# Optimization experiments

Hardware: AMD Instinct MI355X
Metric: run time of the kernel (lower is better)

Reference implementation:

```python
import jax, jax.numpy as jnp
import numpy as np

EPS = 1e-5

def _ln(t, w, b):
    m = t.mean(-1, keepdims=True)
    xc = t - m
    var = (xc * xc).mean(-1, keepdims=True)
    return xc * jax.lax.rsqrt(var + EPS) * w + b

def _rope(q, k, cos, sin):
    # q,k: [B,H,N,hd]; cos,sin: [N, hd//2]
    def rot(t):
        B, H, N, hd = t.shape
        tp = t.reshape(B, H, N, hd // 2, 2)
        r, i = tp[..., 0], tp[..., 1]
        c = cos[None, None, :, :]
        s = sin[None, None, :, :]
        orr = r * c - i * s
        oii = r * s + i * c
        return jnp.stack([orr, oii], axis=-1).reshape(B, H, N, hd)
    return rot(q), rot(k)

def setup_inputs() -> dict:
    key = jax.random.key(0)
    B, N1, N2, D, H = 2, 2048, 256, 1024, 16
    hd = D // H
    ks = jax.random.split(key, 8)
    def w(k, shape):
        return jax.random.normal(k, shape, jnp.float32) * 0.02
    x = jax.random.normal(ks[0], (B, N1, D), jnp.float32)
    c = jax.random.normal(ks[1], (B, N2, D), jnp.float32)
    # rotary tables
    t = jnp.arange(N1, dtype=jnp.float32)
    inv_freq = 1.0 / (10000.0 ** (jnp.arange(0, hd, 2, dtype=jnp.float32) / hd))
    ang = jnp.outer(t, inv_freq)  # [N1, hd//2]
    return dict(
        x=x, c=c,
        freqs_cos=jnp.cos(ang), freqs_sin=jnp.sin(ang),
        W_qkv1=w(ks[2], (D, 3 * D)), b_qkv1=jnp.zeros(3 * D, jnp.float32),
        W_qkv2=w(ks[3], (D, 3 * D)), b_qkv2=jnp.zeros(3 * D, jnp.float32),
        qn1_w=jnp.ones(hd, jnp.float32), qn1_b=jnp.zeros(hd, jnp.float32),
        kn1_w=jnp.ones(hd, jnp.float32), kn1_b=jnp.zeros(hd, jnp.float32),
        qn2_w=jnp.ones(hd, jnp.float32), qn2_b=jnp.zeros(hd, jnp.float32),
        kn2_w=jnp.ones(hd, jnp.float32), kn2_b=jnp.zeros(hd, jnp.float32),
        W_proj1=w(ks[4], (D, D)), b_proj1=jnp.zeros(D, jnp.float32),
        W_proj2=w(ks[5], (D, D)), b_proj2=jnp.zeros(D, jnp.float32),
        pre_x=0,
    )

def reference(x, c, freqs_cos, freqs_sin,
              W_qkv1, b_qkv1, W_qkv2, b_qkv2,
              qn1_w, qn1_b, kn1_w, kn1_b,
              qn2_w, qn2_b, kn2_w, kn2_b,
              W_proj1, b_proj1, W_proj2, b_proj2, pre_x):
    B, N1, D = x.shape
    N2 = c.shape[1]
    H = 16
    hd = D // H
    scale = hd ** -0.5

    def split_heads(qkv):
        q, k, v = jnp.split(qkv, 3, axis=-1)
        f = lambda t: t.reshape(B, -1, H, hd).transpose(0, 2, 1, 3)
        return f(q), f(k), f(v)

    q1, k1, v1 = split_heads(x @ W_qkv1 + b_qkv1)
    q1 = _ln(q1, qn1_w, qn1_b)
    k1 = _ln(k1, kn1_w, kn1_b)
    if pre_x:
        qr, kr = _rope(q1[:, :, pre_x:], k1[:, :, pre_x:], freqs_cos, freqs_sin)
        q1 = jnp.concatenate([q1[:, :, :pre_x], qr], axis=2)
        k1 = jnp.concatenate([k1[:, :, :pre_x], kr], axis=2)
    else:
        q1, k1 = _rope(q1, k1, freqs_cos, freqs_sin)

    q2, k2, v2 = split_heads(c @ W_qkv2 + b_qkv2)
    q2 = _ln(q2, qn2_w, qn2_b)
    k2 = _ln(k2, kn2_w, kn2_b)

    q = jnp.concatenate([q1, q2], axis=2)
    k = jnp.concatenate([k1, k2], axis=2)
    v = jnp.concatenate([v1, v2], axis=2)

    scores = jnp.einsum('bhqd,bhkd->bhqk', q, k) * scale
    attn = jax.nn.softmax(scores, axis=-1)
    o = jnp.einsum('bhqk,bhkd->bhqd', attn, v)  # [B,H,N,hd]
    o = o.transpose(0, 2, 1, 3).reshape(B, N1 + N2, D)

    x_out = o[:, :N1] @ W_proj1 + b_proj1
    c_out = o[:, N1:] @ W_proj2 + b_proj2
    return (x_out, c_out)
```

## Files before the change

### kernel.cpp

```cpp
#include <hip/hip_runtime.h>
#include <hip/hip_bf16.h>
#include <stdint.h>

typedef __attribute__((ext_vector_type(8))) short short8;
typedef __attribute__((ext_vector_type(4))) short bf4;
typedef __attribute__((ext_vector_type(4))) float f32x4;

#define B_ 2
#define N1 2048
#define N2 256
#define NT 2304
#define D_ 1024
#define H_ 16
#define HD 64
#define QSCALE 0.18033688011112042f
#define RESCALE_THR 8.0f

static __device__ __forceinline__ float bf2f(short s){
  union { unsigned int u; float f; } u;
  u.u = ((unsigned int)(unsigned short)s) << 16;
  return u.f;
}
static __device__ __forceinline__ short f2bf(float f){
  union { float f; unsigned int u; } v; v.f = f;
  unsigned int u = v.u;
  unsigned int lsb = (u >> 16) & 1u;
  u += 0x7fffu + lsb;
  return (short)(u >> 16);
}
static __device__ __forceinline__ unsigned int cvtpk2(float a, float b){
  union { __hip_bfloat162 h; unsigned int u; } cv;
  cv.h = __float22bfloat162_rn(make_float2(a, b));
  return cv.u;
}

static __device__ __forceinline__ float fexp2(float x){
#if __has_builtin(__builtin_amdgcn_exp2f)
  return __builtin_amdgcn_exp2f(x);
#else
  return exp2f(x);
#endif
}

static __device__ __forceinline__ void gload16(const void* g, void* l){
  __builtin_amdgcn_global_load_lds(
      (const __attribute__((address_space(1))) void*)g,
      (__attribute__((address_space(3))) void*)l, 16, 0, 0);
}

static __device__ __forceinline__ int swz(int row, int chunk){
  return (row << 6) + ((chunk ^ (row & 7)) << 3);
}

__global__ __launch_bounds__(256) void k_cvt_all(const float* __restrict__ x,
                                                 const float* __restrict__ c,
                                                 short* __restrict__ out){
  int i = (blockIdx.x * 256 + threadIdx.x) * 8;
  const float* in = (i < 4194304) ? (x + i) : (c + (i - 4194304));
  float4 a = *(const float4*)(in);
  float4 b = *(const float4*)(in + 4);
  short8 o;
  o[0]=f2bf(a.x); o[1]=f2bf(a.y); o[2]=f2bf(a.z); o[3]=f2bf(a.w);
  o[4]=f2bf(b.x); o[5]=f2bf(b.y); o[6]=f2bf(b.z); o[7]=f2bf(b.w);
  *(short8*)(out + i) = o;
}

__global__ __launch_bounds__(256) void k_transpose_w4(
    const float* __restrict__ Wq1, const float* __restrict__ Wq2,
    const float* __restrict__ Wp1, const float* __restrict__ Wp2,
    short* __restrict__ Wt1, short* __restrict__ Wt2,
    short* __restrict__ Wtp1, short* __restrict__ Wtp2){
  const int id = blockIdx.x;
  const float* W; short* Wt; int N; int bx, by;
  if (id < 768)      { W = Wq1; Wt = Wt1;  N = 3072; bx = id % 48;          by = id / 48; }
  else if (id < 1536){ W = Wq2; Wt = Wt2;  N = 3072; bx = (id-768) % 48;    by = (id-768) / 48; }
  else if (id < 1792){ W = Wp1; Wt = Wtp1; N = 1024; bx = (id-1536) % 16;   by = (id-1536) / 16; }
  else               { W = Wp2; Wt = Wtp2; N = 1024; bx = (id-1792) % 16;   by = (id-1792) / 16; }
  const int K = 1024;
  __shared__ float tl[64][65];
  const int n0 = bx * 64, k0 = by * 64;
  const int t = threadIdx.x, r = t >> 2, c = (t & 3) * 16;
  const float* src = W + (size_t)(k0 + r) * N + n0 + c;
  #pragma unroll
  for (int i = 0; i < 16; i += 4){
    float4 v = *(const float4*)(src + i);
    tl[r][c+i] = v.x; tl[r][c+i+1] = v.y; tl[r][c+i+2] = v.z; tl[r][c+i+3] = v.w;
  }
  __syncthreads();
  short8 o0, o1;
  #pragma unroll
  for (int i = 0; i < 8; i++) o0[i] = f2bf(tl[c+i][r]);
  #pragma unroll
  for (int i = 0; i < 8; i++) o1[i] = f2bf(tl[c+8+i][r]);
  short* dst = Wt + (size_t)(n0 + r) * K + k0 + c;
  *(short8*)(dst)     = o0;
  *(short8*)(dst + 8) = o1;
}

template<int OUT_BF16>
__global__ __launch_bounds__(256) void k_gemm_bt(const short* __restrict__ A,
                                                 const short* __restrict__ Bt,
                                                 const short* __restrict__ Bt2,
                                                 const float* __restrict__ bias,
                                                 const float* __restrict__ bias2,
                                                 void* __restrict__ Cp,
                                                 int N, int K, int Msplit){
  __shared__ __align__(16) short As[128*32];
  __shared__ __align__(16) short Bs[128*32];
  const int t = threadIdx.x;
  const int w = t >> 6, l = t & 63;
  const int lc = l & 15, g = l >> 4;
  const int gx = gridDim.x;
  const int nb = gx * gridDim.y;
  const int bid = blockIdx.y * gx + blockIdx.x;
  const int nbid = (bid & 7) * (nb >> 3) + (bid >> 3);
  const int tm = (nbid / gx) * 128, tn = (nbid % gx) * 128;
  const int wm = (w >> 1) * 64, wn = (w & 1) * 64;

  const short* Bsel = (tm < Msplit) ? Bt : Bt2;
  const float* bsel = (tm < Msplit) ? bias : bias2;

  const int r0 = w*32 + (l >> 2);
  const int r1 = r0 + 16;
  const int cb = (l & 3) * 16;

  const char* Ag0 = (const char*)(A + (size_t)(tm + r0) * K) + cb;
  const char* Ag1 = (const char*)(A + (size_t)(tm + r1) * K) + cb;
  const char* Bg0 = (const char*)(Bsel + (size_t)(tn + r0) * K) + cb;
  const char* Bg1 = (const char*)(Bsel + (size_t)(tn + r1) * K) + cb;
  char* Al0 = (char*)As + (w*2  )*1024;
  char* Al1 = (char*)As + (w*2+1)*1024;
  char* Bl0 = (char*)Bs + (w*2  )*1024;
  char* Bl1 = (char*)Bs + (w*2+1)*1024;

  f32x4 acc[4][4];
  #pragma unroll
  for (int m=0;m<4;m++){
    #pragma unroll
    for (int n=0;n<4;n++){ acc[m][n][0]=0.f; acc[m][n][1]=0.f; acc[m][n][2]=0.f; acc[m][n][3]=0.f; }
  }

  for (int k0 = 0; k0 < K; k0 += 32){
    const int kb = k0 * 2;
    gload16(Ag0 + kb, Al0);
    gload16(Ag1 + kb, Al1);
    gload16(Bg0 + kb, Bl0);
    gload16(Bg1 + kb, Bl1);
    __syncthreads();
    short8 af[4], bfr[4];
    #pragma unroll
    for (int m=0;m<4;m++) af[m]  = *(const short8*)(As + (wm + m*16 + lc)*32 + g*8);
    #pragma unroll
    for (int n=0;n<4;n++) bfr[n] = *(const short8*)(Bs + (wn + n*16 + lc)*32 + g*8);
    #pragma unroll
    for (int m=0;m<4;m++){
      #pragma unroll
      for (int n=0;n<4;n++)
        acc[m][n] = __builtin_amdgcn_mfma_f32_16x16x32_bf16(af[m], bfr[n], acc[m][n], 0, 0, 0);
    }
    __syncthreads();
  }

  #pragma unroll
  for (int n=0;n<4;n++){
    const int col = tn + wn + n*16 + lc;
    const float bv = bsel[col];
    #pragma unroll
    for (int m=0;m<4;m++){
      const int row = tm + wm + m*16 + g*4;
      #pragma unroll
      for (int r=0;r<4;r++){
        float v = acc[m][n][r] + bv;
        if (OUT_BF16) ((short*)Cp)[(size_t)(row + r)*N + col] = f2bf(v);
        else          ((float*)Cp)[(size_t)(row + r)*N + col] = v;
      }
    }
  }
}

__global__ __launch_bounds__(256) void k_lnrope(const short* __restrict__ qkv,
    const float* __restrict__ qw, const float* __restrict__ qb,
    const float* __restrict__ kw, const float* __restrict__ kb,
    const float* __restrict__ fcos, const float* __restrict__ fsin,
    short* __restrict__ Qo, short* __restrict__ Ko, short* __restrict__ Vo,
    int Nseq, int posoff, int use_rope){
  const int wv = (blockIdx.x * 256 + threadIdx.x) >> 6;
  const int l = threadIdx.x & 63;
  const int h = wv % H_;
  const int n = (wv / H_) % Nseq;
  const int b = wv / (H_ * Nseq);
  const size_t ibase = ((size_t)(b * Nseq + n)) * 3072 + h * 64 + l;
  float q = bf2f(qkv[ibase]);
  float k = bf2f(qkv[ibase + 1024]);
  short v = qkv[ibase + 2048];

  float mu = q;
  #pragma unroll
  for (int mk = 1; mk < 64; mk <<= 1) mu += __shfl_xor(mu, mk, 64);
  mu *= (1.f/64.f);
  float dq = q - mu;
  float var = dq * dq;
  #pragma unroll
  for (int mk = 1; mk < 64; mk <<= 1) var += __shfl_xor(var, mk, 64);
  var *= (1.f/64.f);
  float qn = dq * rsqrtf(var + 1e-5f) * qw[l] + qb[l];

  float muk = k;
  #pragma unroll
  for (int mk = 1; mk < 64; mk <<= 1) muk += __shfl_xor(muk, mk, 64);
  muk *= (1.f/64.f);
  float dk = k - muk;
  float vark = dk * dk;
  #pragma unroll
  for (int mk = 1; mk < 64; mk <<= 1) vark += __shfl_xor(vark, mk, 64);
  vark *= (1.f/64.f);
  float kn = dk * rsqrtf(vark + 1e-5f) * kw[l] + kb[l];

  if (use_rope){
    float cv = fcos[(size_t)n * 32 + (l >> 1)];
    float sv = fsin[(size_t)n * 32 + (l >> 1)];
    float qp = __shfl_xor(qn, 1, 64);
    float kp = __shfl_xor(kn, 1, 64);
    qn = (l & 1) ? (qp * sv + qn * cv) : (qn * cv - qp * sv);
    kn = (l & 1) ? (kp * sv + kn * cv) : (kn * cv - kp * sv);
  }
  qn *= QSCALE;
  const size_t obase = ((size_t)(b * H_ + h) * NT + posoff + n) * HD + l;
  Qo[obase] = f2bf(qn);
  Ko[obase] = f2bf(kn);
  Vo[obase] = v;
}

__global__ __launch_bounds__(256) void k_transpose_v(const short* __restrict__ V,
                                                     short* __restrict__ Vt){
  __shared__ short tl[64][72];
  const int blk = blockIdx.x;
  const int bh = blk / 36;
  const int n0 = (blk % 36) * 64;
  const int t = threadIdx.x, r = t >> 2, c = (t & 3) * 16;
  const short* src = V + ((size_t)bh * NT + n0 + r) * HD + c;
  short8 v0 = *(const short8*)(src);
  short8 v1 = *(const short8*)(src + 8);
  #pragma unroll
  for (int i=0;i<8;i++){ tl[r][c+i] = v0[i]; tl[r][c+8+i] = v1[i]; }
  __syncthreads();
  short8 o0, o1;
  #pragma unroll
  for (int i=0;i<8;i++){ o0[i] = tl[c+i][r]; o1[i] = tl[c+8+i][r]; }
  short* dst = Vt + ((size_t)bh * HD + r) * NT + n0 + c;
  *(short8*)dst       = o0;
  *(short8*)(dst + 8) = o1;
}

__global__ __launch_bounds__(512) void k_attn(const short* __restrict__ Q,
                                              const short* __restrict__ Kg,
                                              const short* __restrict__ Vt,
                                              short* __restrict__ o1,
                                              short* __restrict__ o2){
  __shared__ __align__(16) short Kl[2][4096];
  __shared__ __align__(16) short Vl[2][4096];
  __shared__ __align__(16) short Ps[8][1024];
  const int t = threadIdx.x, w = t >> 6, l = t & 63;
  const int lc = l & 15, g = l >> 4;
  const int blk = blockIdx.x;
  const int ch = blk & 7, ii = blk >> 3;
  const int bh = ch * 4 + (ii / 18);
  const int qt = ii % 18;
  const int b = bh >> 4, hh = bh & 15;
  const int q0 = qt * 128 + w * 16;
  const short* Qb = Q  + (size_t)bh * NT * HD;
  const short* Kb = Kg + (size_t)bh * NT * HD;
  const short* Vb = Vt + (size_t)bh * HD * NT;

  short8 qf0 = *(const short8*)(Qb + (size_t)(q0 + lc) * HD + g*8);
  short8 qf1 = *(const short8*)(Qb + (size_t)(q0 + lc) * HD + g*8 + 32);

  const int sr = t >> 3, c0 = t & 7;
  const short* Kgp = Kb + (size_t)sr * HD + c0 * 8;
  const short* Vgp = Vb + (size_t)sr * NT + c0 * 8;
  const int w0 = swz(sr, c0);

  float mcur = -1e30f, lcur = 0.f;
  f32x4 oacc[4];
  #pragma unroll
  for (int j=0;j<4;j++){ oacc[j][0]=0.f; oacc[j][1]=0.f; oacc[j][2]=0.f; oacc[j][3]=0.f; }

  {
    short8 k0 = *(const short8*)(Kgp);
    short8 v0 = *(const short8*)(Vgp);
    *(short8*)&Kl[0][w0] = k0;
    *(short8*)&Vl[0][w0] = v0;
  }
  __syncthreads();

  for (int ti = 0; ti < 36; ++ti){
    const int cur = ti & 1;
    short8 kn0, vn0;
    if (ti < 35){
      kn0 = *(const short8*)(Kgp + (size_t)(ti + 1) * 64 * HD);
      vn0 = *(const short8*)(Vgp + (ti + 1) * 64);
    }
    f32x4 s[4];
    __builtin_amdgcn_s_setprio(1);
    #pragma unroll
    for (int j=0;j<4;j++){
      const int row = j*16 + lc;
      short8 k0 = *(const short8*)(&Kl[cur][swz(row, g)]);
      short8 k1 = *(const short8*)(&Kl[cur][swz(row, g + 4)]);
      f32x4 a; a[0]=0.f; a[1]=0.f; a[2]=0.f; a[3]=0.f;
      a = __builtin_amdgcn_mfma_f32_16x16x32_bf16(k0, qf0, a, 0, 0, 0);
      a = __builtin_amdgcn_mfma_f32_16x16x32_bf16(k1, qf1, a, 0, 0, 0);
      s[j] = a;
    }
    __builtin_amdgcn_s_setprio(0);
    float t0 = fmaxf(fmaxf(s[0][0], s[0][1]), fmaxf(s[0][2], s[0][3]));
    float t1 = fmaxf(fmaxf(s[1][0], s[1][1]), fmaxf(s[1][2], s[1][3]));
    float t2 = fmaxf(fmaxf(s[2][0], s[2][1]), fmaxf(s[2][2], s[2][3]));
    float t3 = fmaxf(fmaxf(s[3][0], s[3][1]), fmaxf(s[3][2], s[3][3]));
    float tmx = fmaxf(fmaxf(t0, t1), fmaxf(t2, t3));
    tmx = fmaxf(tmx, __shfl_xor(tmx, 16, 64));
    tmx = fmaxf(tmx, __shfl_xor(tmx, 32, 64));
    float mn = mcur;
    if (__any(tmx > mcur + RESCALE_THR)){
      mn = fmaxf(mcur, tmx);
      const float fsc = fexp2(mcur - mn);
      mcur = mn;
      lcur *= fsc;
      #pragma unroll
      for (int j=0;j<4;j++){
        oacc[j][0] *= fsc; oacc[j][1] *= fsc; oacc[j][2] *= fsc; oacc[j][3] *= fsc;
      }
    }
    float p[4][4];
    #pragma unroll
    for (int j=0;j<4;j++){
      p[j][0] = fexp2(s[j][0] - mn);
      p[j][1] = fexp2(s[j][1] - mn);
      p[j][2] = fexp2(s[j][2] - mn);
      p[j][3] = fexp2(s[j][3] - mn);
    }
    float rs = ((p[0][0]+p[0][1])+(p[0][2]+p[0][3]))
             + ((p[1][0]+p[1][1])+(p[1][2]+p[1][3]))
             + ((p[2][0]+p[2][1])+(p[2][2]+p[2][3]))
             + ((p[3][0]+p[3][1])+(p[3][2]+p[3][3]));
    rs += __shfl_xor(rs, 16, 64);
    rs += __shfl_xor(rs, 32, 64);
    lcur += rs;
    #pragma unroll
    for (int j=0;j<4;j++){
      const int si = (lc << 6) + (((2*j + (g >> 1)) ^ (lc & 7)) << 3) + (g & 1) * 4;
      unsigned int* dst = (unsigned int*)&Ps[w][si];
      dst[0] = cvtpk2(p[j][0], p[j][1]);
      dst[1] = cvtpk2(p[j][2], p[j][3]);
    }
    #pragma unroll
    for (int kk=0;kk<2;kk++){
      short8 pa = *(const short8*)(&Ps[w][swz(lc, 4*kk + g)]);
      __builtin_amdgcn_s_setprio(1);
      #pragma unroll
      for (int jd=0;jd<4;jd++){
        short8 vb = *(const short8*)(&Vl[cur][swz(lc + 16*jd, 4*kk + g)]);
        oacc[jd] = __builtin_amdgcn_mfma_f32_16x16x32_bf16(vb, pa, oacc[jd], 0, 0, 0);
      }
      __builtin_amdgcn_s_setprio(0);
    }
    if (ti < 35){
      *(short8*)&Kl[cur ^ 1][w0] = kn0;
      *(short8*)&Vl[cur ^ 1][w0] = vn0;
    }
    __syncthreads();
  }

  const float inv = 1.0f / lcur;
  const int qi = q0 + lc;
  short* obase = (qi < N1) ? (o1 + ((size_t)b * N1 + qi) * D_)
                           : (o2 + ((size_t)b * N2 + (qi - N1)) * D_);
  #pragma unroll
  for (int jd=0;jd<4;jd++){
    bf4 ov;
    #pragma unroll
    for (int r=0;r<4;r++) ov[r] = f2bf(oacc[jd][r] * inv);
    *(bf4*)(obase + hh*64 + 16*jd + 4*g) = ov;
  }
}

extern "C" void kernel_launch(void* const* d_in, const int* in_sizes, int n_in,
                              void* d_out, int out_size, void* d_ws, size_t ws_size,
                              hipStream_t stream){
  const float* x    = (const float*)d_in[0];
  const float* c    = (const float*)d_in[1];
  const float* fc   = (const float*)d_in[2];
  const float* fs   = (const float*)d_in[3];
  const float* Wq1  = (const float*)d_in[4];
  const float* bq1  = (const float*)d_in[5];
  const float* Wq2  = (const float*)d_in[6];
  const float* bq2  = (const float*)d_in[7];
  const float* qn1w = (const float*)d_in[8];
  const float* qn1b = (const float*)d_in[9];
  const float* kn1w = (const float*)d_in[10];
  const float* kn1b = (const float*)d_in[11];
  const float* qn2w = (const float*)d_in[12];
  const float* qn2b = (const float*)d_in[13];
  const float* kn2w = (const float*)d_in[14];
  const float* kn2b = (const float*)d_in[15];
  const float* Wp1  = (const float*)d_in[16];
  const float* bp1  = (const float*)d_in[17];
  const float* Wp2  = (const float*)d_in[18];
  const float* bp2  = (const float*)d_in[19];
  float* out = (float*)d_out;

  char* ws = (char*)d_ws;
  short* xb   = (short*)(ws);
  short* Wt1  = (short*)(ws + 9437184);
  short* Wt2  = (short*)(ws + 15728640);
  short* Wtp1 = (short*)(ws + 22020096);
  short* Wtp2 = (short*)(ws + 24117248);
  short* qkv1 = (short*)(ws + 26214400);
  short* qkv2 = (short*)(ws + 51380224);
  short* Qb   = (short*)(ws + 54525952);
  short* Kb   = (short*)(ws + 63963136);
  short* Vb   = (short*)(ws + 73400320);
  short* o1   = (short*)(ws + 26214400);
  short* Vtb  = (short*)(ws + 26214400 + 9437184);

  k_cvt_all<<<2304, 256, 0, stream>>>(x, c, xb);
  k_transpose_w4<<<2048, 256, 0, stream>>>(Wq1, Wq2, Wp1, Wp2, Wt1, Wt2, Wtp1, Wtp2);

  k_gemm_bt<1><<<dim3(24,36), 256, 0, stream>>>(xb, Wt1, Wt2, bq1, bq2, qkv1, 3072, 1024, 4096);

  k_lnrope<<<16384, 256, 0, stream>>>(qkv1, qn1w, qn1b, kn1w, kn1b, fc, fs, Qb, Kb, Vb, 2048, 0, 1);
  k_lnrope<<<2048,  256, 0, stream>>>(qkv2, qn2w, qn2b, kn2w, kn2b, fc, fs, Qb, Kb, Vb,  256, 2048, 0);

  k_transpose_v<<<1152, 256, 0, stream>>>(Vb, Vtb);
  k_attn<<<576, 512, 0, stream>>>(Qb, Kb, Vtb, o1, o1 + 4194304);

  k_gemm_bt<0><<<dim3(8,36), 256, 0, stream>>>(o1, Wtp1, Wtp2, bp1, bp2, out, 1024, 1024, 4096);
}
```

Before: 217.1 us.

## Fuse per-head LayerNorm, RoPE and V transpose into QKV GEMM epilogue

```diff
diff --git a/kernel.cpp b/kernel.cpp
--- a/kernel.cpp
+++ b/kernel.cpp
@@ -97,14 +97,15 @@
   *(short8*)(dst + 8) = o1;
 }
 
-template<int OUT_BF16>
-__global__ __launch_bounds__(256) void k_gemm_bt(const short* __restrict__ A,
-                                                 const short* __restrict__ Bt,
-                                                 const short* __restrict__ Bt2,
-                                                 const float* __restrict__ bias,
-                                                 const float* __restrict__ bias2,
-                                                 void* __restrict__ Cp,
-                                                 int N, int K, int Msplit){
+__global__ __launch_bounds__(256) void k_gemm_qkv(const short* __restrict__ A,
+    const short* __restrict__ Bt, const short* __restrict__ Bt2,
+    const float* __restrict__ bias, const float* __restrict__ bias2,
+    const float* __restrict__ qn1w, const float* __restrict__ qn1b,
+    const float* __restrict__ kn1w, const float* __restrict__ kn1b,
+    const float* __restrict__ qn2w, const float* __restrict__ qn2b,
+    const float* __restrict__ kn2w, const float* __restrict__ kn2b,
+    const float* __restrict__ fcos, const float* __restrict__ fsin,
+    short* __restrict__ Qo, short* __restrict__ Ko, short* __restrict__ Vto){
   __shared__ __align__(16) short As[128*32];
   __shared__ __align__(16) short Bs[128*32];
   const int t = threadIdx.x;
@@ -116,9 +117,11 @@
   const int nbid = (bid & 7) * (nb >> 3) + (bid >> 3);
   const int tm = (nbid / gx) * 128, tn = (nbid % gx) * 128;
   const int wm = (w >> 1) * 64, wn = (w & 1) * 64;
-
-  const short* Bsel = (tm < Msplit) ? Bt : Bt2;
-  const float* bsel = (tm < Msplit) ? bias : bias2;
+  const int K = 1024;
+  const bool s1 = (tm < 4096);
+
+  const short* Bsel = s1 ? Bt : Bt2;
+  const float* bsel = s1 ? bias : bias2;
 
   const int r0 = w*32 + (l >> 2);
   const int r1 = r0 + 16;
@@ -163,93 +166,164 @@
 
   #pragma unroll
   for (int n=0;n<4;n++){
+    const float bv = bsel[tn + wn + n*16 + lc];
+    #pragma unroll
+    for (int m=0;m<4;m++){
+      acc[m][n][0] += bv; acc[m][n][1] += bv; acc[m][n][2] += bv; acc[m][n][3] += bv;
+    }
+  }
+
+  const int colbase = tn + wn;
+  const int grp = colbase >> 10;
+  const int hh = (colbase & 1023) >> 6;
+
+  if (grp == 2){
+    #pragma unroll
+    for (int m=0;m<4;m++){
+      const int row0 = tm + wm + m*16 + g*4;
+      const int bb  = s1 ? (row0 >> 11) : ((row0 - 4096) >> 8);
+      const int pos = s1 ? (row0 & 2047) : (2048 + ((row0 - 4096) & 255));
+      short* vbase = Vto + (size_t)(bb*16 + hh) * 64 * NT + pos;
+      #pragma unroll
+      for (int n=0;n<4;n++){
+        const int d = n*16 + lc;
+        bf4 ov;
+        #pragma unroll
+        for (int r=0;r<4;r++) ov[r] = f2bf(acc[m][n][r]);
+        *(bf4*)(vbase + (size_t)d * NT) = ov;
+      }
+    }
+    return;
+  }
+
+  const float* lnw = (grp == 0) ? (s1 ? qn1w : qn2w) : (s1 ? kn1w : kn2w);
+  const float* lnb = (grp == 0) ? (s1 ? qn1b : qn2b) : (s1 ? kn1b : kn2b);
+  short* outp = (grp == 0) ? Qo : Ko;
+  float wv_[4], bv_[4];
+  #pragma unroll
+  for (int n=0;n<4;n++){ wv_[n] = lnw[n*16 + lc]; bv_[n] = lnb[n*16 + lc]; }
+
+  #pragma unroll
+  for (int m=0;m<4;m++){
+    float mu[4], rv[4];
+    #pragma unroll
+    for (int r=0;r<4;r++){
+      float s  = (acc[m][0][r] + acc[m][1][r]) + (acc[m][2][r] + acc[m][3][r]);
+      float sq = (acc[m][0][r]*acc[m][0][r] + acc[m][1][r]*acc[m][1][r])
+               + (acc[m][2][r]*acc[m][2][r] + acc[m][3][r]*acc[m][3][r]);
+      s  += __shfl_xor(s, 1, 64);  sq += __shfl_xor(sq, 1, 64);
+      s  += __shfl_xor(s, 2, 64);  sq += __shfl_xor(sq, 2, 64);
+      s  += __shfl_xor(s, 4, 64);  sq += __shfl_xor(sq, 4, 64);
+      s  += __shfl_xor(s, 8, 64);  sq += __shfl_xor(sq, 8, 64);
+      mu[r] = s * (1.f/64.f);
+      const float var = sq * (1.f/64.f) - mu[r]*mu[r];
+      rv[r] = rsqrtf(var + 1e-5f);
+    }
+    const int row0 = tm + wm + m*16 + g*4;
+    const int bb  = s1 ? (row0 >> 11) : ((row0 - 4096) >> 8);
+    const int pos0 = s1 ? (row0 & 2047) : (2048 + ((row0 - 4096) & 255));
+    short* obase = outp + ((size_t)(bb*16 + hh) * NT + pos0) * 64;
+    #pragma unroll
+    for (int n=0;n<4;n++){
+      float xh[4];
+      #pragma unroll
+      for (int r=0;r<4;r++) xh[r] = (acc[m][n][r] - mu[r]) * rv[r] * wv_[n] + bv_[n];
+      if (s1){
+        #pragma unroll
+        for (int r=0;r<4;r++){
+          const size_t fi = (size_t)(pos0 + r) * 32 + n*8 + (lc >> 1);
+          const float cv = fcos[fi];
+          const float sv = fsin[fi];
+          const float p = __shfl_xor(xh[r], 1, 64);
+          xh[r] = (lc & 1) ? (p*sv + xh[r]*cv) : (xh[r]*cv - p*sv);
+        }
+      }
+      if (grp == 0){
+        #pragma unroll
+        for (int r=0;r<4;r++) xh[r] *= QSCALE;
+      }
+      const int d = n*16 + lc;
+      #pragma unroll
+      for (int r=0;r<4;r++) obase[(size_t)r * 64 + d] = f2bf(xh[r]);
+    }
+  }
+}
+
+__global__ __launch_bounds__(256) void k_gemm_proj(const short* __restrict__ A,
+                                                   const short* __restrict__ Bt,
+                                                   const short* __restrict__ Bt2,
+                                                   const float* __restrict__ bias,
+                                                   const float* __restrict__ bias2,
+                                                   float* __restrict__ Cp,
+                                                   int N, int K, int Msplit){
+  __shared__ __align__(16) short As[128*32];
+  __shared__ __align__(16) short Bs[128*32];
+  const int t = threadIdx.x;
+  const int w = t >> 6, l = t & 63;
+  const int lc = l & 15, g = l >> 4;
+  const int gx = gridDim.x;
+  const int nb = gx * gridDim.y;
+  const int bid = blockIdx.y * gx + blockIdx.x;
+  const int nbid = (bid & 7) * (nb >> 3) + (bid >> 3);
+  const int tm = (nbid / gx) * 128, tn = (nbid % gx) * 128;
+  const int wm = (w >> 1) * 64, wn = (w & 1) * 64;
+
+  const short* Bsel = (tm < Msplit) ? Bt : Bt2;
+  const float* bsel = (tm < Msplit) ? bias : bias2;
+
+  const int r0 = w*32 + (l >> 2);
+  const int r1 = r0 + 16;
+  const int cb = (l & 3) * 16;
+
+  const char* Ag0 = (const char*)(A + (size_t)(tm + r0) * K) + cb;
+  const char* Ag1 = (const char*)(A + (size_t)(tm + r1) * K) + cb;
+  const char* Bg0 = (const char*)(Bsel + (size_t)(tn + r0) * K) + cb;
+  const char* Bg1 = (const char*)(Bsel + (size_t)(tn + r1) * K) + cb;
+  char* Al0 = (char*)As + (w*2  )*1024;
+  char* Al1 = (char*)As + (w*2+1)*1024;
+  char* Bl0 = (char*)Bs + (w*2  )*1024;
+  char* Bl1 = (char*)Bs + (w*2+1)*1024;
+
+  f32x4 acc[4][4];
+  #pragma unroll
+  for (int m=0;m<4;m++){
+    #pragma unroll
+    for (int n=0;n<4;n++){ acc[m][n][0]=0.f; acc[m][n][1]=0.f; acc[m][n][2]=0.f; acc[m][n][3]=0.f; }
+  }
+
+  for (int k0 = 0; k0 < K; k0 += 32){
+    const int kb = k0 * 2;
+    gload16(Ag0 + kb, Al0);
+    gload16(Ag1 + kb, Al1);
+    gload16(Bg0 + kb, Bl0);
+    gload16(Bg1 + kb, Bl1);
+    __syncthreads();
+    short8 af[4], bfr[4];
+    #pragma unroll
+    for (int m=0;m<4;m++) af[m]  = *(const short8*)(As + (wm + m*16 + lc)*32 + g*8);
+    #pragma unroll
+    for (int n=0;n<4;n++) bfr[n] = *(const short8*)(Bs + (wn + n*16 + lc)*32 + g*8);
+    #pragma unroll
+    for (int m=0;m<4;m++){
+      #pragma unroll
+      for (int n=0;n<4;n++)
+        acc[m][n] = __builtin_amdgcn_mfma_f32_16x16x32_bf16(af[m], bfr[n], acc[m][n], 0, 0, 0);
+    }
+    __syncthreads();
+  }
+
+  #pragma unroll
+  for (int n=0;n<4;n++){
     const int col = tn + wn + n*16 + lc;
     const float bv = bsel[col];
     #pragma unroll
     for (int m=0;m<4;m++){
       const int row = tm + wm + m*16 + g*4;
       #pragma unroll
-      for (int r=0;r<4;r++){
-        float v = acc[m][n][r] + bv;
-        if (OUT_BF16) ((short*)Cp)[(size_t)(row + r)*N + col] = f2bf(v);
-        else          ((float*)Cp)[(size_t)(row + r)*N + col] = v;
-      }
-    }
-  }
-}
-
-__global__ __launch_bounds__(256) void k_lnrope(const short* __restrict__ qkv,
-    const float* __restrict__ qw, const float* __restrict__ qb,
-    const float* __restrict__ kw, const float* __restrict__ kb,
-    const float* __restrict__ fcos, const float* __restrict__ fsin,
-    short* __restrict__ Qo, short* __restrict__ Ko, short* __restrict__ Vo,
-    int Nseq, int posoff, int use_rope){
-  const int wv = (blockIdx.x * 256 + threadIdx.x) >> 6;
-  const int l = threadIdx.x & 63;
-  const int h = wv % H_;
-  const int n = (wv / H_) % Nseq;
-  const int b = wv / (H_ * Nseq);
-  const size_t ibase = ((size_t)(b * Nseq + n)) * 3072 + h * 64 + l;
-  float q = bf2f(qkv[ibase]);
-  float k = bf2f(qkv[ibase + 1024]);
-  short v = qkv[ibase + 2048];
-
-  float mu = q;
-  #pragma unroll
-  for (int mk = 1; mk < 64; mk <<= 1) mu += __shfl_xor(mu, mk, 64);
-  mu *= (1.f/64.f);
-  float dq = q - mu;
-  float var = dq * dq;
-  #pragma unroll
-  for (int mk = 1; mk < 64; mk <<= 1) var += __shfl_xor(var, mk, 64);
-  var *= (1.f/64.f);
-  float qn = dq * rsqrtf(var + 1e-5f) * qw[l] + qb[l];
-
-  float muk = k;
-  #pragma unroll
-  for (int mk = 1; mk < 64; mk <<= 1) muk += __shfl_xor(muk, mk, 64);
-  muk *= (1.f/64.f);
-  float dk = k - muk;
-  float vark = dk * dk;
-  #pragma unroll
-  for (int mk = 1; mk < 64; mk <<= 1) vark += __shfl_xor(vark, mk, 64);
-  vark *= (1.f/64.f);
-  float kn = dk * rsqrtf(vark + 1e-5f) * kw[l] + kb[l];
-
-  if (use_rope){
-    float cv = fcos[(size_t)n * 32 + (l >> 1)];
-    float sv = fsin[(size_t)n * 32 + (l >> 1)];
-    float qp = __shfl_xor(qn, 1, 64);
-    float kp = __shfl_xor(kn, 1, 64);
-    qn = (l & 1) ? (qp * sv + qn * cv) : (qn * cv - qp * sv);
-    kn = (l & 1) ? (kp * sv + kn * cv) : (kn * cv - kp * sv);
-  }
-  qn *= QSCALE;
-  const size_t obase = ((size_t)(b * H_ + h) * NT + posoff + n) * HD + l;
-  Qo[obase] = f2bf(qn);
-  Ko[obase] = f2bf(kn);
-  Vo[obase] = v;
-}
-
-__global__ __launch_bounds__(256) void k_transpose_v(const short* __restrict__ V,
-                                                     short* __restrict__ Vt){
-  __shared__ short tl[64][72];
-  const int blk = blockIdx.x;
-  const int bh = blk / 36;
-  const int n0 = (blk % 36) * 64;
-  const int t = threadIdx.x, r = t >> 2, c = (t & 3) * 16;
-  const short* src = V + ((size_t)bh * NT + n0 + r) * HD + c;
-  short8 v0 = *(const short8*)(src);
-  short8 v1 = *(const short8*)(src + 8);
-  #pragma unroll
-  for (int i=0;i<8;i++){ tl[r][c+i] = v0[i]; tl[r][c+8+i] = v1[i]; }
-  __syncthreads();
-  short8 o0, o1;
-  #pragma unroll
-  for (int i=0;i<8;i++){ o0[i] = tl[c+i][r]; o1[i] = tl[c+8+i][r]; }
-  short* dst = Vt + ((size_t)bh * HD + r) * NT + n0 + c;
-  *(short8*)dst       = o0;
-  *(short8*)(dst + 8) = o1;
+      for (int r=0;r<4;r++)
+        Cp[(size_t)(row + r)*N + col] = acc[m][n][r] + bv;
+    }
+  }
 }
 
 __global__ __launch_bounds__(512) void k_attn(const short* __restrict__ Q,
@@ -415,24 +489,18 @@
   short* Wt2  = (short*)(ws + 15728640);
   short* Wtp1 = (short*)(ws + 22020096);
   short* Wtp2 = (short*)(ws + 24117248);
-  short* qkv1 = (short*)(ws + 26214400);
-  short* qkv2 = (short*)(ws + 51380224);
+  short* o1   = (short*)(ws + 26214400);
+  short* Vtb  = (short*)(ws + 26214400 + 9437184);
   short* Qb   = (short*)(ws + 54525952);
   short* Kb   = (short*)(ws + 63963136);
-  short* Vb   = (short*)(ws + 73400320);
-  short* o1   = (short*)(ws + 26214400);
-  short* Vtb  = (short*)(ws + 26214400 + 9437184);
 
   k_cvt_all<<<2304, 256, 0, stream>>>(x, c, xb);
   k_transpose_w4<<<2048, 256, 0, stream>>>(Wq1, Wq2, Wp1, Wp2, Wt1, Wt2, Wtp1, Wtp2);
 
-  k_gemm_bt<1><<<dim3(24,36), 256, 0, stream>>>(xb, Wt1, Wt2, bq1, bq2, qkv1, 3072, 1024, 4096);
-
-  k_lnrope<<<16384, 256, 0, stream>>>(qkv1, qn1w, qn1b, kn1w, kn1b, fc, fs, Qb, Kb, Vb, 2048, 0, 1);
-  k_lnrope<<<2048,  256, 0, stream>>>(qkv2, qn2w, qn2b, kn2w, kn2b, fc, fs, Qb, Kb, Vb,  256, 2048, 0);
-
-  k_transpose_v<<<1152, 256, 0, stream>>>(Vb, Vtb);
+  k_gemm_qkv<<<dim3(24,36), 256, 0, stream>>>(xb, Wt1, Wt2, bq1, bq2,
+      qn1w, qn1b, kn1w, kn1b, qn2w, qn2b, kn2w, kn2b, fc, fs, Qb, Kb, Vtb);
+
   k_attn<<<576, 512, 0, stream>>>(Qb, Kb, Vtb, o1, o1 + 4194304);
 
-  k_gemm_bt<0><<<dim3(8,36), 256, 0, stream>>>(o1, Wtp1, Wtp2, bp1, bp2, out, 1024, 1024, 4096);
-}
+  k_gemm_proj<<<dim3(8,36), 256, 0, stream>>>(o1, Wtp1, Wtp2, bp1, bp2, out, 1024, 1024, 4096);
+}
```

Result: faster. 189.4 us (-12.7%).
